# Kernel optimization log

Measured on AMD Instinct MI355X. Metric: run time of the kernel, lower is better.

Reference implementation:

```python
import jax, jax.numpy as jnp
import numpy as np

N = 50000
E = 800000
IN_CH = 256
HID = 64
HEADS = 8
OUT_CH = 16
NEG_SLOPE = 0.2


def _glorot(key, shape):
    fan_in, fan_out = shape[0], shape[-1]
    lim = float(np.sqrt(6.0 / (fan_in + fan_out)))
    return jax.random.uniform(key, shape, jnp.float32, -lim, lim)


def setup_inputs() -> dict:
    key = jax.random.key(0)
    ks = jax.random.split(key, 12)
    x = jax.random.normal(ks[0], (N, IN_CH), jnp.float32)
    edge_index = jax.random.randint(ks[1], (2, E), 0, N, jnp.int64)
    # layer 1: GATConv(256 -> 64, heads=8)
    W1 = _glorot(ks[2], (IN_CH, HEADS * HID))
    a_src1 = _glorot(ks[3], (HEADS, HID))
    a_dst1 = _glorot(ks[4], (HEADS, HID))
    b1 = jnp.zeros((HEADS * HID,), jnp.float32)
    # layer 2: GATConv(512 -> 16, heads=1, concat=False)
    W2 = _glorot(ks[5], (HEADS * HID, OUT_CH))
    a_src2 = _glorot(ks[6], (1, OUT_CH))
    a_dst2 = _glorot(ks[7], (1, OUT_CH))
    b2 = jnp.zeros((OUT_CH,), jnp.float32)
    return {"x": x, "edge_index": edge_index, "W1": W1, "a_src1": a_src1,
            "a_dst1": a_dst1, "b1": b1, "W2": W2, "a_src2": a_src2,
            "a_dst2": a_dst2, "b2": b2}


def _gat_conv(x, src, dst, W, a_src, a_dst, bias, heads, out_ch, concat):
    n = x.shape[0]
    h = (x @ W).reshape(n, heads, out_ch)            # [N,H,C]
    alpha_s = jnp.einsum('nhc,hc->nh', h, a_src)      # [N,H]
    alpha_d = jnp.einsum('nhc,hc->nh', h, a_dst)
    e = alpha_s[src] + alpha_d[dst]                   # [E,H]
    e = jnp.where(e > 0, e, NEG_SLOPE * e)            # leaky_relu
    # segment softmax over incoming edges of each dst node
    e_max = jax.ops.segment_max(e, dst, num_segments=n)
    e_max = jnp.where(jnp.isfinite(e_max), e_max, 0.0)
    p = jnp.exp(e - e_max[dst])                       # [E,H]
    denom = jax.ops.segment_sum(p, dst, num_segments=n)
    alpha = p / (denom[dst] + 1e-16)                  # [E,H]
    msg = h[src] * alpha[:, :, None]                  # [E,H,C]
    out = jax.ops.segment_sum(msg, dst, num_segments=n)  # [N,H,C]
    if concat:
        out = out.reshape(n, heads * out_ch)
    else:
        out = out.mean(axis=1)
    return out + bias


def reference(x, edge_index, W1, a_src1, a_dst1, b1, W2, a_src2, a_dst2, b2):
    n = x.shape[0]
    loops = jnp.arange(n, dtype=edge_index.dtype)
    ei = jnp.concatenate([edge_index, jnp.stack([loops, loops])], axis=1)
    src, dst = ei[0], ei[1]
    h = _gat_conv(x, src, dst, W1, a_src1, a_dst1, b1, HEADS, HID, True)
    h = jax.nn.elu(h)
    out = _gat_conv(h, src, dst, W2, a_src2, a_dst2, b2, 1, OUT_CH, False)
    return jax.nn.log_softmax(out, axis=-1)
```

## Files before the change

kernel.cpp:

```cpp
#include <hip/hip_runtime.h>
#include <math.h>

#define IN_CH 256
#define HID 64
#define HEADS 8
#define F1 512
#define OUT_CH 16
#define NEG 0.2f
#define NBUCK 16

typedef __attribute__((ext_vector_type(8))) short bf16x8;
typedef __attribute__((ext_vector_type(4))) float f32x4;
typedef __attribute__((ext_vector_type(2))) float f32x2;

__device__ __forceinline__ float bflo(unsigned int v) {
  unsigned int t = v << 16; return __builtin_bit_cast(float, t);
}
__device__ __forceinline__ float bfhi(unsigned int v) {
  unsigned int t = v & 0xFFFF0000u; return __builtin_bit_cast(float, t);
}
__device__ __forceinline__ unsigned short f2bf(float f) {
  unsigned int u = __builtin_bit_cast(unsigned int, f);
  u += 0x7FFFu + ((u >> 16) & 1u);
  return (unsigned short)(u >> 16);
}
__device__ __forceinline__ void gld_lds16(const void* g, void* l) {
  __builtin_amdgcn_global_load_lds(
      (const __attribute__((address_space(1))) unsigned int*)g,
      (__attribute__((address_space(3))) unsigned int*)l, 16, 0, 0);
}


__global__ void prep_kernel(const int* __restrict__ ei, int E, int N,
                            int* counts16,
                            const float* __restrict__ W1, unsigned short* __restrict__ W1R,
                            const float* __restrict__ W2, unsigned short* __restrict__ W2T) {
  int idx = blockIdx.x * blockDim.x + threadIdx.x;
  int ET = E + N;
  if (idx < ET) {
    int src, dst;
    if (idx < E) { src = ei[idx]; dst = ei[E + idx]; }
    else         { src = idx - E; dst = idx - E; }
    atomicAdd(&counts16[dst * NBUCK + (src >> 12)], 1);
  }
  if (idx < F1 * IN_CH) {
    int n = idx >> 8, k = idx & 255;
    int r = (((k >> 5) * 4 + ((k >> 3) & 3)) * 512 + n) * 8 + (k & 7);
    W1R[r] = f2bf(W1[k * F1 + n]);
  }
  if (idx < OUT_CH * F1) {
    int n = idx >> 9, k = idx & 511;
    W2T[idx] = f2bf(W2[k * OUT_CH + n]);
  }
}

__global__ __launch_bounds__(1024) void scan1_kernel(const int* __restrict__ counts16,
                                                     int* __restrict__ offsets16,
                                                     int* __restrict__ bsum, int n16) {
  __shared__ int lds[1024];
  int t = threadIdx.x;
  int base = blockIdx.x * 16384 + t * 16;
  int v[16];
  int tot = 0;
  if (base < n16) {
    #pragma unroll
    for (int k = 0; k < 4; ++k) {
      int4 c = *(const int4*)(counts16 + base + k * 4);
      v[k * 4 + 0] = c.x; v[k * 4 + 1] = c.y; v[k * 4 + 2] = c.z; v[k * 4 + 3] = c.w;
    }
    #pragma unroll
    for (int k = 0; k < 16; ++k) { int c = v[k]; v[k] = tot; tot += c; }
  } else {
    #pragma unroll
    for (int k = 0; k < 16; ++k) v[k] = 0;
  }
  lds[t] = tot;
  __syncthreads();
  for (int off = 1; off < 1024; off <<= 1) {
    int u = (t >= off) ? lds[t - off] : 0;
    __syncthreads();
    lds[t] += u;
    __syncthreads();
  }
  int excl = lds[t] - tot;
  if (base < n16) {
    #pragma unroll
    for (int k = 0; k < 4; ++k) {
      int4 o = make_int4(excl + v[k * 4], excl + v[k * 4 + 1],
                         excl + v[k * 4 + 2], excl + v[k * 4 + 3]);
      *(int4*)(offsets16 + base + k * 4) = o;
    }
  }
  if (t == 1023) bsum[blockIdx.x] = lds[1023];
}

__global__ __launch_bounds__(1024) void scan3b_kernel(int* __restrict__ offsets16,
                                                      const int* __restrict__ bsum,
                                                      int nb, int n16) {
  __shared__ int s_pre, s_tot;
  int t = threadIdx.x;
  if (t < 64) {
    int v = (t < nb) ? bsum[t] : 0;
    int vp = (t < (int)blockIdx.x) ? v : 0;
    #pragma unroll
    for (int off = 1; off < 64; off <<= 1) {
      vp += __shfl_xor(vp, off);
      v  += __shfl_xor(v, off);
    }
    if (t == 0) { s_pre = vp; s_tot = v; }
  }
  __syncthreads();
  int base = blockIdx.x * 16384 + t * 16;
  if (base < n16) {
    #pragma unroll
    for (int k = 0; k < 4; ++k) {
      int4 o = *(const int4*)(offsets16 + base + k * 4);
      o.x += s_pre; o.y += s_pre; o.z += s_pre; o.w += s_pre;
      *(int4*)(offsets16 + base + k * 4) = o;
    }
  }
  if (blockIdx.x == 0 && t == 0) offsets16[n16] = s_tot;
}

__global__ void fill_kernel(const int* __restrict__ ei, int E, int N,
                            int* offsets16, int* __restrict__ csr_src) {
  int e = blockIdx.x * blockDim.x + threadIdx.x;
  int ET = E + N;
  if (e >= ET) return;
  int src, dst;
  if (e < E) { src = ei[e]; dst = ei[E + e]; }
  else       { src = e - E; dst = e - E; }
  int key = dst * NBUCK + (src >> 12);
  int pos = atomicAdd(&offsets16[key], 1);
  csr_src[pos] = src;
}

__device__ __forceinline__ void seg_lookup(const int* __restrict__ offA, int node,
                                           int& beg, int& deg) {
  beg = (node == 0) ? 0 : offA[node * NBUCK - 1];
  deg = offA[node * NBUCK + NBUCK - 1] - beg;
}


__global__ __launch_bounds__(512) void gemm1_mfma(const float* __restrict__ X,
                                                  const unsigned short* __restrict__ W1R,
                                                  const float* __restrict__ Asrc,
                                                  const float* __restrict__ Adst,
                                                  unsigned char* __restrict__ C,
                                                  float2* __restrict__ aad1, int M) {
  __shared__ __align__(16) short sB[4 * 512 * 8];
  int tid = threadIdx.x, w = tid >> 6, l = tid & 63;
  int wm = (w >> 2) * 32;
  int wn = (w & 3) * 128;
  int bm = blockIdx.x * 64;
  f32x4 acc[2][8];
  #pragma unroll
  for (int mi = 0; mi < 2; ++mi)
    #pragma unroll
    for (int nj = 0; nj < 8; ++nj) acc[mi][nj] = (f32x4){0.f, 0.f, 0.f, 0.f};
  int kslot = l >> 4;
  for (int kb = 0; kb < 8; ++kb) {
    __syncthreads();
    const unsigned short* src = W1R + kb * 16384;
    #pragma unroll
    for (int i = 0; i < 4; ++i)
      gld_lds16(src + (size_t)(i * 512 + tid) * 8, (char*)sB + (i * 512 + tid) * 16);
    bf16x8 af[2];
    int kbase = kb * 32 + kslot * 8;
    #pragma unroll
    for (int mi = 0; mi < 2; ++mi) {
      int r = bm + wm + mi * 16 + (l & 15);
      if (r >= M) r = M - 1;
      const float* ap = X + (size_t)r * IN_CH + kbase;
      float4 a0 = *(const float4*)ap;
      float4 a1 = *(const float4*)(ap + 4);
      unsigned int u0, u1, u2, u3;
      asm("v_cvt_pk_bf16_f32 %0, %1, %2" : "=v"(u0) : "v"(a0.x), "v"(a0.y));
      asm("v_cvt_pk_bf16_f32 %0, %1, %2" : "=v"(u1) : "v"(a0.z), "v"(a0.w));
      asm("v_cvt_pk_bf16_f32 %0, %1, %2" : "=v"(u2) : "v"(a1.x), "v"(a1.y));
      asm("v_cvt_pk_bf16_f32 %0, %1, %2" : "=v"(u3) : "v"(a1.z), "v"(a1.w));
      int4 pk = make_int4(u0, u1, u2, u3);
      af[mi] = __builtin_bit_cast(bf16x8, pk);
    }
    __syncthreads();
    #pragma unroll
    for (int nj = 0; nj < 8; ++nj) {
      int n = wn + nj * 16 + (l & 15);
      bf16x8 bf = *(const bf16x8*)&sB[(kslot * 512 + n) * 8];
      acc[0][nj] = __builtin_amdgcn_mfma_f32_16x16x32_bf16(af[0], bf, acc[0][nj], 0, 0, 0);
      acc[1][nj] = __builtin_amdgcn_mfma_f32_16x16x32_bf16(af[1], bf, acc[1][nj], 0, 0, 0);
    }
  }
  float asv[8], adv[8];
  #pragma unroll
  for (int nj = 0; nj < 8; ++nj) {
    int c = wn + nj * 16 + (l & 15);
    asv[nj] = Asrc[c]; adv[nj] = Adst[c];
  }
  int h0 = (w & 3) * 2;
  #pragma unroll
  for (int mi = 0; mi < 2; ++mi) {
    #pragma unroll
    for (int j = 0; j < 4; ++j) {
      int r = bm + wm + mi * 16 + (l >> 4) * 4 + j;
      bool ok = (r < M);
      if (ok) {
        #pragma unroll
        for (int njp = 0; njp < 4; ++njp) {
          int u = __builtin_amdgcn_cvt_pk_fp8_f32(acc[mi][2 * njp][j],
                                                  acc[mi][2 * njp + 1][j], 0, false);
          int c0 = wn + (2 * njp) * 16 + (l & 15);
          C[(size_t)r * F1 + c0]      = (unsigned char)u;
          C[(size_t)r * F1 + c0 + 16] = (unsigned char)(u >> 8);
        }
      }
      float sA = 0.f, dA = 0.f, sB2 = 0.f, dB2 = 0.f;
      #pragma unroll
      for (int nj = 0; nj < 4; ++nj) {
        float v = acc[mi][nj][j];
        sA += v * asv[nj]; dA += v * adv[nj];
      }
      #pragma unroll
      for (int nj = 4; nj < 8; ++nj) {
        float v = acc[mi][nj][j];
        sB2 += v * asv[nj]; dB2 += v * adv[nj];
      }
      #pragma unroll
      for (int off = 1; off < 16; off <<= 1) {
        sA += __shfl_xor(sA, off); dA += __shfl_xor(dA, off);
        sB2 += __shfl_xor(sB2, off); dB2 += __shfl_xor(dB2, off);
      }
      if (ok && (l & 15) == 0) {
        aad1[r * HEADS + h0]     = make_float2(sA, dA);
        aad1[r * HEADS + h0 + 1] = make_float2(sB2, dB2);
      }
    }
  }
}


__global__ __launch_bounds__(256) void aggr1_kernel(const uint2* __restrict__ h1q,
                                                    const float2* __restrict__ aad1,
                                                    const int* __restrict__ offA,
                                                    const int* __restrict__ csr_src,
                                                    const float* __restrict__ b1,
                                                    uint4* __restrict__ out1v, int N) {
  int tid = threadIdx.x;
  int w = tid >> 6, l = tid & 63;
  int b = blockIdx.x;
  int nwg = gridDim.x;
  int q = nwg >> 3, r = nwg & 7;
  int xcd = b & 7, bi = b >> 3;
  int swz = (xcd < r) ? (xcd * (q + 1) + bi) : (r * (q + 1) + (xcd - r) * q + bi);
  int node = swz * 4 + w;
  if (node >= N) return;
  int beg, deg;
  seg_lookup(offA, node, beg, deg);
  int he = l & 7;
  int hc = l >> 3;
  float adv = aad1[node * HEADS + he].y;
  float pden = 0.f;
  float acc[8] = {};
  int e = l >> 3;
  for (int c0 = 0; c0 < deg; c0 += 8) {
    int cnt = min(8, deg - c0);
    int s8 = 0;
    float p8 = 0.f;
    if (e < cnt) {
      s8 = csr_src[beg + c0 + e];
      float2 sd = aad1[s8 * HEADS + he];
      float ev = sd.x + adv;
      ev = (ev > 0.f) ? ev : NEG * ev;
      p8 = __expf(ev);
      pden += p8;
    }
    if (cnt == 8) {
      int ss[8]; float qq[8];
      #pragma unroll
      for (int j = 0; j < 8; ++j) {
        ss[j] = __shfl(s8, j * 8);
        qq[j] = __shfl(p8, j * 8 + hc);
      }
      uint2 v[8];
      #pragma unroll
      for (int j = 0; j < 8; ++j) v[j] = h1q[(size_t)ss[j] * 64 + l];
      #pragma unroll
      for (int j = 0; j < 8; ++j) {
        float p = qq[j];
        f32x2 f0 = __builtin_amdgcn_cvt_pk_f32_fp8(v[j].x, false);
        f32x2 f1 = __builtin_amdgcn_cvt_pk_f32_fp8(v[j].x, true);
        f32x2 f2 = __builtin_amdgcn_cvt_pk_f32_fp8(v[j].y, false);
        f32x2 f3 = __builtin_amdgcn_cvt_pk_f32_fp8(v[j].y, true);
        acc[0] += p * f0[0]; acc[1] += p * f0[1];
        acc[2] += p * f1[0]; acc[3] += p * f1[1];
        acc[4] += p * f2[0]; acc[5] += p * f2[1];
        acc[6] += p * f3[0]; acc[7] += p * f3[1];
      }
    } else {
      for (int j = 0; j < cnt; ++j) {
        int s = __shfl(s8, j * 8);
        float p = __shfl(p8, j * 8 + hc);
        uint2 v = h1q[(size_t)s * 64 + l];
        f32x2 f0 = __builtin_amdgcn_cvt_pk_f32_fp8(v.x, false);
        f32x2 f1 = __builtin_amdgcn_cvt_pk_f32_fp8(v.x, true);
        f32x2 f2 = __builtin_amdgcn_cvt_pk_f32_fp8(v.y, false);
        f32x2 f3 = __builtin_amdgcn_cvt_pk_f32_fp8(v.y, true);
        acc[0] += p * f0[0]; acc[1] += p * f0[1];
        acc[2] += p * f1[0]; acc[3] += p * f1[1];
        acc[4] += p * f2[0]; acc[5] += p * f2[1];
        acc[6] += p * f3[0]; acc[7] += p * f3[1];
      }
    }
  }
  pden += __shfl_xor(pden, 8);
  pden += __shfl_xor(pden, 16);
  pden += __shfl_xor(pden, 32);
  float den = __shfl(pden, hc) + 1e-16f;
  float4 bv0 = *(const float4*)&b1[l * 8];
  float4 bv1 = *(const float4*)&b1[l * 8 + 4];
  float o[8];
  o[0] = acc[0] / den + bv0.x; o[1] = acc[1] / den + bv0.y;
  o[2] = acc[2] / den + bv0.z; o[3] = acc[3] / den + bv0.w;
  o[4] = acc[4] / den + bv1.x; o[5] = acc[5] / den + bv1.y;
  o[6] = acc[6] / den + bv1.z; o[7] = acc[7] / den + bv1.w;
  #pragma unroll
  for (int i = 0; i < 8; ++i) o[i] = (o[i] > 0.f) ? o[i] : expm1f(o[i]);
  uint4 ov;
  ov.x = (unsigned int)f2bf(o[0]) | ((unsigned int)f2bf(o[1]) << 16);
  ov.y = (unsigned int)f2bf(o[2]) | ((unsigned int)f2bf(o[3]) << 16);
  ov.z = (unsigned int)f2bf(o[4]) | ((unsigned int)f2bf(o[5]) << 16);
  ov.w = (unsigned int)f2bf(o[6]) | ((unsigned int)f2bf(o[7]) << 16);
  out1v[(size_t)node * 64 + l] = ov;
}


__global__ __launch_bounds__(256) void gemm2_mfma(const unsigned short* __restrict__ A,
                                                  const unsigned short* __restrict__ W2T,
                                                  const float* __restrict__ a_src2,
                                                  const float* __restrict__ a_dst2,
                                                  float* __restrict__ t2,
                                                  float2* __restrict__ aad2, int M) {
  __shared__ __align__(16) short sW[16 * 512];
  int tid = threadIdx.x, w = tid >> 6, l = tid & 63;
  for (int i = tid; i < 1024; i += 256) ((uint4*)sW)[i] = ((const uint4*)W2T)[i];
  __syncthreads();
  int bm = blockIdx.x * 128 + w * 32;
  f32x4 acc[2];
  acc[0] = (f32x4){0.f, 0.f, 0.f, 0.f};
  acc[1] = (f32x4){0.f, 0.f, 0.f, 0.f};
  int rl = l & 15;
  int koff = (l >> 4) * 8;
  int r0 = bm + rl;       if (r0 >= M) r0 = M - 1;
  int r1 = bm + 16 + rl;  if (r1 >= M) r1 = M - 1;
  const unsigned short* a0p = A + (size_t)r0 * F1 + koff;
  const unsigned short* a1p = A + (size_t)r1 * F1 + koff;
  #pragma unroll
  for (int k0 = 0; k0 < F1; k0 += 32) {
    bf16x8 bfv = *(const bf16x8*)&sW[rl * 512 + k0 + koff];
    bf16x8 af0 = *(const bf16x8*)(a0p + k0);
    bf16x8 af1 = *(const bf16x8*)(a1p + k0);
    acc[0] = __builtin_amdgcn_mfma_f32_16x16x32_bf16(af0, bfv, acc[0], 0, 0, 0);
    acc[1] = __builtin_amdgcn_mfma_f32_16x16x32_bf16(af1, bfv, acc[1], 0, 0, 0);
  }
  float asv = a_src2[rl], adv = a_dst2[rl];
  #pragma unroll
  for (int mi = 0; mi < 2; ++mi) {
    #pragma unroll
    for (int j = 0; j < 4; ++j) {
      int r = bm + mi * 16 + (l >> 4) * 4 + j;
      float val = acc[mi][j];
      float s = val * asv, d = val * adv;
      s += __shfl_xor(s, 1); s += __shfl_xor(s, 2); s += __shfl_xor(s, 4); s += __shfl_xor(s, 8);
      d += __shfl_xor(d, 1); d += __shfl_xor(d, 2); d += __shfl_xor(d, 4); d += __shfl_xor(d, 8);
      if (r < M) {
        t2[(size_t)r * OUT_CH + rl] = val;
        if (rl == 0) aad2[r] = make_float2(s, d);
      }
    }
  }
}


__global__ __launch_bounds__(256) void aggr2_kernel(const float* __restrict__ t2,
                                                    const float2* __restrict__ aad2,
                                                    const int* __restrict__ offA,
                                                    const int* __restrict__ csr_src,
                                                    const float* __restrict__ b2,
                                                    float* __restrict__ out, int N) {
  int tid = threadIdx.x;
  int node = blockIdx.x * 4 + (tid >> 6);
  int lane = tid & 63;
  if (node >= N) return;
  int beg, deg;
  seg_lookup(offA, node, beg, deg);
  float ad = aad2[node].y;
  float acc = 0.f, den = 0.f;
  int eg = lane >> 4, c = lane & 15;
  for (int base = 0; base < deg; base += 8) {
    int j1 = base + eg;
    int j2 = base + 4 + eg;
    bool ok1 = j1 < deg, ok2 = j2 < deg;
    int s1 = csr_src[beg + (ok1 ? j1 : 0)];
    int s2 = csr_src[beg + (ok2 ? j2 : 0)];
    float2 m1 = aad2[s1];
    float2 m2 = aad2[s2];
    float t1v = t2[(size_t)s1 * OUT_CH + c];
    float t2v = t2[(size_t)s2 * OUT_CH + c];
    float e1 = m1.x + ad;
    e1 = (e1 > 0.f) ? e1 : NEG * e1;
    float p1 = ok1 ? __expf(e1) : 0.f;
    float e2 = m2.x + ad;
    e2 = (e2 > 0.f) ? e2 : NEG * e2;
    float p2 = ok2 ? __expf(e2) : 0.f;
    acc += p1 * t1v + p2 * t2v;
    if (c == 0) den += p1 + p2;
  }
  acc += __shfl_xor(acc, 16); acc += __shfl_xor(acc, 32);
  den += __shfl_xor(den, 16); den += __shfl_xor(den, 32);
  den = __shfl(den, 0);
  float val = acc / (den + 1e-16f) + b2[c];
  float mx = val;
  #pragma unroll
  for (int off = 1; off < 16; off <<= 1) mx = fmaxf(mx, __shfl_xor(mx, off));
  float ex = __expf(val - mx);
  float se = ex;
  #pragma unroll
  for (int off = 1; off < 16; off <<= 1) se += __shfl_xor(se, off);
  float ls = val - mx - logf(se);
  if (lane < 16) out[(size_t)node * OUT_CH + lane] = ls;
}


extern "C" void kernel_launch(void* const* d_in, const int* in_sizes, int n_in,
                              void* d_out, int out_size, void* d_ws, size_t ws_size,
                              hipStream_t stream) {
  const float* x      = (const float*)d_in[0];
  const int*   ei     = (const int*)d_in[1];
  const float* W1     = (const float*)d_in[2];
  const float* a_src1 = (const float*)d_in[3];
  const float* a_dst1 = (const float*)d_in[4];
  const float* b1     = (const float*)d_in[5];
  const float* W2     = (const float*)d_in[6];
  const float* a_src2 = (const float*)d_in[7];
  const float* a_dst2 = (const float*)d_in[8];
  const float* b2     = (const float*)d_in[9];
  float* out = (float*)d_out;

  int N = in_sizes[0] / IN_CH;
  int E = in_sizes[1] / 2;
  int ET = E + N;
  int n16 = N * NBUCK;

  char* w = (char*)d_ws;
  auto alloc = [&](size_t bytes) -> void* {
    void* p = (void*)w;
    w += (bytes + 255) & ~(size_t)255;
    return p;
  };
  unsigned char*  h1b   = (unsigned char*)alloc((size_t)N * F1);
  unsigned short* out1b = (unsigned short*)alloc((size_t)N * F1 * 2);
  unsigned short* w1r   = (unsigned short*)alloc((size_t)F1 * IN_CH * 2);
  unsigned short* w2t   = (unsigned short*)alloc((size_t)OUT_CH * F1 * 2);
  float* aad1  = (float*)alloc((size_t)N * HEADS * 8);
  float* t2    = (float*)alloc((size_t)N * OUT_CH * 4);
  float* aad2  = (float*)alloc((size_t)N * 8);
  int* counts16 = (int*)alloc((size_t)n16 * 4);
  int* offsets16 = (int*)alloc((size_t)(n16 + 1) * 4);
  int* bsum    = (int*)alloc(256 * 4);
  int* csr_src = (int*)alloc((size_t)ET * 4);

  int nb = (n16 + 16383) / 16384;

  hipMemsetAsync(counts16, 0, (size_t)n16 * 4, stream);
  prep_kernel<<<(ET + 255) / 256, 256, 0, stream>>>(ei, E, N, counts16, W1, w1r, W2, w2t);
  scan1_kernel<<<nb, 1024, 0, stream>>>(counts16, offsets16, bsum, n16);
  scan3b_kernel<<<nb, 1024, 0, stream>>>(offsets16, bsum, nb, n16);
  fill_kernel<<<(ET + 255) / 256, 256, 0, stream>>>(ei, E, N, offsets16, csr_src);

  gemm1_mfma<<<(N + 63) / 64, 512, 0, stream>>>(x, w1r, a_src1, a_dst1, h1b,
                                                (float2*)aad1, N);
  aggr1_kernel<<<(N + 3) / 4, 256, 0, stream>>>((const uint2*)h1b, (const float2*)aad1,
                                                offsets16, csr_src, b1, (uint4*)out1b, N);
  gemm2_mfma<<<(N + 127) / 128, 256, 0, stream>>>(out1b, w2t, a_src2, a_dst2, t2,
                                                  (float2*)aad2, N);
  aggr2_kernel<<<(N + 3) / 4, 256, 0, stream>>>(t2, (const float2*)aad2, offsets16, csr_src,
                                                b2, out, N);
}
```

Baseline: 284.9 us.

## Read GEMM1 weights directly from global and pack aggregation FMAs

GEMM1 no longer stages W1 tiles into LDS with async global-to-LDS loads and two barriers per k-step; each wave instead reads its bf16 B fragments straight from global memory, relying on L2/L1 caching of the small weight matrix. The layer-1 aggregation kernel switches its accumulators to float2 vectors so the compiler can emit packed FMA instructions. The GEMM change removes synchronization and LDS traffic but adds redundant global loads across waves and blocks.

```diff
diff --git a/kernel.cpp b/kernel.cpp
--- a/kernel.cpp
+++ b/kernel.cpp
@@ -23,11 +23,6 @@
   unsigned int u = __builtin_bit_cast(unsigned int, f);
   u += 0x7FFFu + ((u >> 16) & 1u);
   return (unsigned short)(u >> 16);
-}
-__device__ __forceinline__ void gld_lds16(const void* g, void* l) {
-  __builtin_amdgcn_global_load_lds(
-      (const __attribute__((address_space(1))) unsigned int*)g,
-      (__attribute__((address_space(3))) unsigned int*)l, 16, 0, 0);
 }
 
 
@@ -148,7 +143,6 @@
                                                   const float* __restrict__ Adst,
                                                   unsigned char* __restrict__ C,
                                                   float2* __restrict__ aad1, int M) {
-  __shared__ __align__(16) short sB[4 * 512 * 8];
   int tid = threadIdx.x, w = tid >> 6, l = tid & 63;
   int wm = (w >> 2) * 32;
   int wn = (w & 3) * 128;
@@ -160,11 +154,6 @@
     for (int nj = 0; nj < 8; ++nj) acc[mi][nj] = (f32x4){0.f, 0.f, 0.f, 0.f};
   int kslot = l >> 4;
   for (int kb = 0; kb < 8; ++kb) {
-    __syncthreads();
-    const unsigned short* src = W1R + kb * 16384;
-    #pragma unroll
-    for (int i = 0; i < 4; ++i)
-      gld_lds16(src + (size_t)(i * 512 + tid) * 8, (char*)sB + (i * 512 + tid) * 16);
     bf16x8 af[2];
     int kbase = kb * 32 + kslot * 8;
     #pragma unroll
@@ -182,11 +171,11 @@
       int4 pk = make_int4(u0, u1, u2, u3);
       af[mi] = __builtin_bit_cast(bf16x8, pk);
     }
-    __syncthreads();
+    const unsigned short* bbase = W1R + (size_t)(kb * 4 + kslot) * 512 * 8;
     #pragma unroll
     for (int nj = 0; nj < 8; ++nj) {
       int n = wn + nj * 16 + (l & 15);
-      bf16x8 bf = *(const bf16x8*)&sB[(kslot * 512 + n) * 8];
+      bf16x8 bf = *(const bf16x8*)(bbase + n * 8);
       acc[0][nj] = __builtin_amdgcn_mfma_f32_16x16x32_bf16(af[0], bf, acc[0][nj], 0, 0, 0);
       acc[1][nj] = __builtin_amdgcn_mfma_f32_16x16x32_bf16(af[1], bf, acc[1][nj], 0, 0, 0);
     }
@@ -260,7 +249,9 @@
   int hc = l >> 3;
   float adv = aad1[node * HEADS + he].y;
   float pden = 0.f;
-  float acc[8] = {};
+  f32x2 acc2[4];
+  #pragma unroll
+  for (int i = 0; i < 4; ++i) acc2[i] = (f32x2){0.f, 0.f};
   int e = l >> 3;
   for (int c0 = 0; c0 < deg; c0 += 8) {
     int cnt = min(8, deg - c0);
@@ -286,29 +277,22 @@
       for (int j = 0; j < 8; ++j) v[j] = h1q[(size_t)ss[j] * 64 + l];
       #pragma unroll
       for (int j = 0; j < 8; ++j) {
-        float p = qq[j];
-        f32x2 f0 = __builtin_amdgcn_cvt_pk_f32_fp8(v[j].x, false);
-        f32x2 f1 = __builtin_amdgcn_cvt_pk_f32_fp8(v[j].x, true);
-        f32x2 f2 = __builtin_amdgcn_cvt_pk_f32_fp8(v[j].y, false);
-        f32x2 f3 = __builtin_amdgcn_cvt_pk_f32_fp8(v[j].y, true);
-        acc[0] += p * f0[0]; acc[1] += p * f0[1];
-        acc[2] += p * f1[0]; acc[3] += p * f1[1];
-        acc[4] += p * f2[0]; acc[5] += p * f2[1];
-        acc[6] += p * f3[0]; acc[7] += p * f3[1];
+        f32x2 p2 = (f32x2){qq[j], qq[j]};
+        acc2[0] += p2 * __builtin_amdgcn_cvt_pk_f32_fp8(v[j].x, false);
+        acc2[1] += p2 * __builtin_amdgcn_cvt_pk_f32_fp8(v[j].x, true);
+        acc2[2] += p2 * __builtin_amdgcn_cvt_pk_f32_fp8(v[j].y, false);
+        acc2[3] += p2 * __builtin_amdgcn_cvt_pk_f32_fp8(v[j].y, true);
       }
     } else {
       for (int j = 0; j < cnt; ++j) {
         int s = __shfl(s8, j * 8);
         float p = __shfl(p8, j * 8 + hc);
         uint2 v = h1q[(size_t)s * 64 + l];
-        f32x2 f0 = __builtin_amdgcn_cvt_pk_f32_fp8(v.x, false);
-        f32x2 f1 = __builtin_amdgcn_cvt_pk_f32_fp8(v.x, true);
-        f32x2 f2 = __builtin_amdgcn_cvt_pk_f32_fp8(v.y, false);
-        f32x2 f3 = __builtin_amdgcn_cvt_pk_f32_fp8(v.y, true);
-        acc[0] += p * f0[0]; acc[1] += p * f0[1];
-        acc[2] += p * f1[0]; acc[3] += p * f1[1];
-        acc[4] += p * f2[0]; acc[5] += p * f2[1];
-        acc[6] += p * f3[0]; acc[7] += p * f3[1];
+        f32x2 p2 = (f32x2){p, p};
+        acc2[0] += p2 * __builtin_amdgcn_cvt_pk_f32_fp8(v.x, false);
+        acc2[1] += p2 * __builtin_amdgcn_cvt_pk_f32_fp8(v.x, true);
+        acc2[2] += p2 * __builtin_amdgcn_cvt_pk_f32_fp8(v.y, false);
+        acc2[3] += p2 * __builtin_amdgcn_cvt_pk_f32_fp8(v.y, true);
       }
     }
   }
@@ -319,10 +303,10 @@
   float4 bv0 = *(const float4*)&b1[l * 8];
   float4 bv1 = *(const float4*)&b1[l * 8 + 4];
   float o[8];
-  o[0] = acc[0] / den + bv0.x; o[1] = acc[1] / den + bv0.y;
-  o[2] = acc[2] / den + bv0.z; o[3] = acc[3] / den + bv0.w;
-  o[4] = acc[4] / den + bv1.x; o[5] = acc[5] / den + bv1.y;
-  o[6] = acc[6] / den + bv1.z; o[7] = acc[7] / den + bv1.w;
+  o[0] = acc2[0][0] / den + bv0.x; o[1] = acc2[0][1] / den + bv0.y;
+  o[2] = acc2[1][0] / den + bv0.z; o[3] = acc2[1][1] / den + bv0.w;
+  o[4] = acc2[2][0] / den + bv1.x; o[5] = acc2[2][1] / den + bv1.y;
+  o[6] = acc2[3][0] / den + bv1.z; o[7] = acc2[3][1] / den + bv1.w;
   #pragma unroll
   for (int i = 0; i < 8; ++i) o[i] = (o[i] > 0.f) ? o[i] : expm1f(o[i]);
   uint4 ov;
```

After: 290.6 us. 2.0% more time.
